# Kernel optimization log

Hardware: AMD Instinct MI355X
Metric: run time of the kernel (lower is better)

## Reference

```python
import jax, jax.numpy as jnp
import numpy as np


def _ortho_matrix(key, d, m):
    # block-orthogonal random matrix with chi-distributed row-norm rescaling
    n_blocks = m // d + (1 if m % d else 0)
    keys = jax.random.split(key, n_blocks + 1)
    blocks = []
    for i in range(m // d):
        q, _ = jnp.linalg.qr(jax.random.normal(keys[i], (d, d), dtype=jnp.float32))
        blocks.append(q)
    rem = m % d
    if rem > 0:
        q, _ = jnp.linalg.qr(jax.random.normal(keys[m // d], (d, d), dtype=jnp.float32))
        blocks.append(q[:, :rem])
    proj = jnp.concatenate(blocks, axis=1)  # [d, m]
    scales = jnp.linalg.norm(jax.random.normal(keys[-1], (m, d), dtype=jnp.float32), axis=1)
    return proj * scales[None, :]


def _feature_map(x, P, eps=1e-6):
    # FAVOR+ positive softmax feature map: [exp(xP - |x|^2/2), exp(-xP - |x|^2/2)]
    proj = x @ P  # [B,N,m]
    xn = 0.5 * jnp.sum(x * x, axis=-1, keepdims=True)
    pos = proj - xn
    neg = -proj - xn
    mx = jnp.maximum(jnp.max(pos, axis=-1, keepdims=True), jnp.max(neg, axis=-1, keepdims=True))
    feats = jnp.concatenate([jnp.exp(pos - mx), jnp.exp(neg - mx)], axis=-1)
    return feats * (2.0 * P.shape[1]) ** -0.5 + eps  # [B,N,2m]


def setup_inputs() -> dict:
    key = jax.random.key(0)
    ks = jax.random.split(key, 16)
    B, C, N = 4, 256, 8192
    da, nb = C // 4, 64
    d_geo, r_geo = 16, 16
    x = jax.random.normal(ks[0], (B, C, N), dtype=jnp.float32)
    pos = jax.random.uniform(ks[1], (B, N, 3), dtype=jnp.float32)
    Wq = jax.random.normal(ks[2], (da, C), dtype=jnp.float32) * (C ** -0.5)
    Wk = jax.random.normal(ks[3], (da, C), dtype=jnp.float32) * (C ** -0.5)
    Wv = jax.random.normal(ks[4], (C, C), dtype=jnp.float32) * (C ** -0.5)
    proj_sm = _ortho_matrix(ks[5], da, nb)  # [da, nb]
    Wg1 = jax.random.normal(ks[6], (d_geo, 3), dtype=jnp.float32) * (3 ** -0.5)
    bg1 = jnp.zeros((d_geo,), dtype=jnp.float32)
    Wg2 = jax.random.normal(ks[7], (d_geo, d_geo), dtype=jnp.float32) * (d_geo ** -0.5)
    bg2 = jnp.zeros((d_geo,), dtype=jnp.float32)
    log_tau = jnp.zeros((), dtype=jnp.float32)
    omega_geo = _ortho_matrix(ks[8], d_geo, r_geo)  # [d_geo, r_geo]
    Wp = jax.random.normal(ks[9], (C, C), dtype=jnp.float32) * (C ** -0.5)
    bn_gamma = jnp.ones((C,), dtype=jnp.float32)
    bn_beta = jnp.zeros((C,), dtype=jnp.float32)
    return {"x": x, "pos": pos, "Wq": Wq, "Wk": Wk, "Wv": Wv, "proj_sm": proj_sm,
            "Wg1": Wg1, "bg1": bg1, "Wg2": Wg2, "bg2": bg2, "log_tau": log_tau,
            "omega_geo": omega_geo, "Wp": Wp, "bn_gamma": bn_gamma, "bn_beta": bn_beta}


def reference(x, pos, Wq, Wk, Wv, proj_sm, Wg1, bg1, Wg2, bg2, log_tau, omega_geo, Wp, bn_gamma, bn_beta):
    eps = 1e-6
    da = Wq.shape[0]
    scale = da ** -0.25
    # 1x1 convs == channel matmuls; transpose to [B,N,*]
    q = jnp.einsum('bcn,oc->bno', x, Wq) * scale
    k = jnp.einsum('bcn,oc->bno', x, Wk) * scale
    v = jnp.einsum('bcn,oc->bno', x, Wv)
    q_p = _feature_map(q, proj_sm, eps)  # [B,N,r_sm]
    k_p = _feature_map(k, proj_sm, eps)
    # GeoRFF: learnable Gaussian RFF on MLP-transformed coordinates
    g = jax.nn.relu(pos @ Wg1.T + bg1) @ Wg2.T + bg2  # [B,N,d_geo]
    tau = jax.nn.softplus(log_tau) + 1e-6
    z = jnp.sqrt(2.0 * tau) * g
    z_proj = z @ omega_geo  # [B,N,r_geo]
    z_norm = 0.5 * jnp.sum(z * z, axis=-1, keepdims=True)
    phi = jnp.exp(z_proj - z_norm) * (omega_geo.shape[1] ** -0.5)  # [B,N,r_geo]
    # outer-product feature combination
    B, N, r_sm = q_p.shape
    r_geo = phi.shape[-1]
    Phi_q = (q_p[..., :, None] * phi[..., None, :]).reshape(B, N, r_sm * r_geo)
    Phi_k = (k_p[..., :, None] * phi[..., None, :]).reshape(B, N, r_sm * r_geo)
    # O(N) linear-attention chain
    kv = jnp.einsum('bnr,bnc->brc', Phi_k, v)         # [B,r,C]
    k_sum = jnp.sum(Phi_k, axis=1)                     # [B,r]
    denom = jnp.einsum('bnr,br->bn', Phi_q, k_sum)[..., None] + eps
    fsa = jnp.einsum('bnr,brc->bnc', Phi_q, kv) / denom  # [B,N,C]
    # offset attention: proj(x - fsa) + x, proj = Conv1x1 -> BN(train stats) -> ReLU
    y = x - jnp.transpose(fsa, (0, 2, 1))  # [B,C,N]
    h = jnp.einsum('bcn,oc->bon', y, Wp)
    mean = jnp.mean(h, axis=(0, 2), keepdims=True)
    var = jnp.var(h, axis=(0, 2), keepdims=True)
    hn = (h - mean) * jax.lax.rsqrt(var + 1e-5) * bn_gamma[None, :, None] + bn_beta[None, :, None]
    return jax.nn.relu(hn) + x
```

## Files before the change

### kernel.cpp

```cpp
#include <hip/hip_runtime.h>
#include <hip/hip_bf16.h>
#include <math.h>

#define BB 4
#define CC 256
#define NN 8192
#define RSM 128
#define RGEO 16

typedef __attribute__((ext_vector_type(8))) short short8v;
typedef __attribute__((ext_vector_type(4))) float f32x4;
typedef __attribute__((ext_vector_type(4))) unsigned int u32x4;

#define MFMA16 __builtin_amdgcn_mfma_f32_16x16x32_bf16

#define P_QP   0ull
#define P_KPT  8388608ull
#define P_PHIR 16777216ull
#define P_PHIT 17825792ull
#define P_XT   18874368ull
#define P_VT   35651584ull
#define P_YNT  35651584ull
#define P_KVT  52428800ull
#define P_KVF  56623104ull
#define P_KSUM 65011712ull
#define P_DEN  65044480ull
#define P_WQK  65175552ull
#define P_WV   65241088ull
#define P_WP   65372160ull
#define P_PSMT 65503232ull
#define P_BN   65511424ull
#define P_H    0ull

__device__ __forceinline__ unsigned short f2bu(float f){
    __hip_bfloat16 h = __float2bfloat16(f);
    return __builtin_bit_cast(unsigned short, h);
}
__device__ __forceinline__ float bu2f(unsigned short u){
    return __builtin_bit_cast(float, ((unsigned int)u) << 16);
}
__device__ __forceinline__ unsigned int pack2(float a, float b){
    return (unsigned int)f2bu(a) | (((unsigned int)f2bu(b)) << 16);
}
__device__ __forceinline__ int swz128(int row, int cb){ return (row*128 + cb) ^ ((row & 7) << 4); }
__device__ __forceinline__ int swz256(int row, int cb){ return (row*256 + cb) ^ ((row & 7) << 4); }

__device__ __forceinline__ void stage64(const unsigned short* __restrict__ g, size_t stride,
                                        char* lds, int t){
    #pragma unroll
    for (int i = 0; i < 2; ++i){
        int id = t + 256*i; int row = id >> 3, q = id & 7;
        short8v v = *(const short8v*)(g + (size_t)row*stride + q*8);
        *(short8v*)(lds + swz128(row, q*16)) = v;
    }
}
__device__ __forceinline__ void stage128(const unsigned short* __restrict__ g, size_t stride,
                                         char* lds, int t){
    #pragma unroll
    for (int i = 0; i < 4; ++i){
        int id = t + 256*i; int row = id >> 3, q = id & 7;
        short8v v = *(const short8v*)(g + (size_t)row*stride + q*8);
        *(short8v*)(lds + swz128(row, q*16)) = v;
    }
}
__device__ __forceinline__ short8v fld(const char* lds, int row, int cb){
    return *(const short8v*)(lds + swz128(row, cb));
}
__device__ __forceinline__ void mfma8(const char* As, const char* Bs, f32x4 acc[2][2],
                                      int wm, int wn, int lr, int lq){
    #pragma unroll
    for (int kk = 0; kk < 2; ++kk){
        short8v a0 = fld(As, wm*32 + lr,      kk*64 + lq*16);
        short8v a1 = fld(As, wm*32 + 16 + lr, kk*64 + lq*16);
        short8v b0 = fld(Bs, wn*32 + lr,      kk*64 + lq*16);
        short8v b1 = fld(Bs, wn*32 + 16 + lr, kk*64 + lq*16);
        acc[0][0] = MFMA16(a0, b0, acc[0][0], 0, 0, 0);
        acc[0][1] = MFMA16(a0, b1, acc[0][1], 0, 0, 0);
        acc[1][0] = MFMA16(a1, b0, acc[1][0], 0, 0, 0);
        acc[1][1] = MFMA16(a1, b1, acc[1][1], 0, 0, 0);
    }
}
__device__ __forceinline__ void mfma16s(const char* As, const char* Bs, f32x4 acc[4][4],
                                        int wm, int wn, int lr, int lq){
    #pragma unroll
    for (int kk = 0; kk < 2; ++kk){
        short8v af[4], bf[4];
        #pragma unroll
        for (int f = 0; f < 4; ++f) af[f] = fld(As, wm*64 + f*16 + lr, kk*64 + lq*16);
        #pragma unroll
        for (int f = 0; f < 4; ++f) bf[f] = fld(Bs, wn*64 + f*16 + lr, kk*64 + lq*16);
        #pragma unroll
        for (int fa = 0; fa < 4; ++fa)
            #pragma unroll
            for (int fb = 0; fb < 4; ++fb)
                acc[fa][fb] = MFMA16(af[fa], bf[fb], acc[fa][fb], 0, 0, 0);
    }
}

__global__ __launch_bounds__(256) void k_prep(const float* __restrict__ Wq, const float* __restrict__ Wk,
    const float* __restrict__ Wv, const float* __restrict__ Wp, const float* __restrict__ Psm,
    unsigned short* __restrict__ Wqk_bf, unsigned short* __restrict__ Wv_bf,
    unsigned short* __restrict__ Wp_bf, unsigned short* __restrict__ Psm_t)
{
    const int tid = blockIdx.x*256 + threadIdx.x;
    const int nth = 64*256;
    for (int i = tid; i < 32768; i += nth){
        int o = i >> 8, c = i & 255;
        Wqk_bf[i] = f2bu(o < 64 ? Wq[o*256 + c] : Wk[(o-64)*256 + c]);
    }
    for (int i = tid; i < 65536; i += nth) Wv_bf[i] = f2bu(Wv[i]);
    for (int i = tid; i < 65536; i += nth) Wp_bf[i] = f2bu(Wp[i]);
    for (int i = tid; i < 4096; i += nth){
        int m = i >> 6, o = i & 63;
        Psm_t[i] = f2bu(Psm[o*64 + m] * 0.35355339059327373f);
    }
}

__global__ __launch_bounds__(256) void k_xt(const float* __restrict__ x, unsigned short* __restrict__ xT)
{
    __shared__ float xs[64][65];
    const int t = threadIdx.x;
    const int b  = blockIdx.x >> 9;
    const int ct = (blockIdx.x >> 7) & 3;
    const int nt = blockIdx.x & 127;
    const int c0 = ct*64, n0 = nt*64;
    #pragma unroll
    for (int i = 0; i < 4; ++i){
        int id = t + 256*i; int row = id >> 4, fq = id & 15;
        f32x4 v = *(const f32x4*)(x + ((size_t)(b*CC + c0 + row))*NN + n0 + fq*4);
        xs[row][fq*4+0] = v[0]; xs[row][fq*4+1] = v[1];
        xs[row][fq*4+2] = v[2]; xs[row][fq*4+3] = v[3];
    }
    __syncthreads();
    #pragma unroll
    for (int i = 0; i < 2; ++i){
        int id = t + 256*i; int n = id >> 3, q = id & 7;
        u32x4 o;
        #pragma unroll
        for (int j2 = 0; j2 < 4; ++j2)
            o[j2] = pack2(xs[q*8 + j2*2][n], xs[q*8 + j2*2+1][n]);
        *(u32x4*)(void*)(xT + ((size_t)(b*NN + n0 + n))*CC + c0 + q*8) = o;
    }
}

__global__ __launch_bounds__(256) void k_wgemm(const unsigned short* __restrict__ A,
    const unsigned short* __restrict__ Bsrc, unsigned short* __restrict__ out, int orows)
{
    __shared__ __align__(16) char As[8192];
    __shared__ __align__(16) char Bs[8192];
    const int t = threadIdx.x;
    const int l = t & 63, w = t >> 6, wm = w >> 1, wn = w & 1, lr = l & 15, lq = l >> 4;
    const int b  = blockIdx.x >> 9;
    const int ct = (blockIdx.x >> 7) & 3;
    const int nt = blockIdx.x & 127;
    const int c0 = ct*64, n0 = nt*64;

    f32x4 acc[2][2] = {};
    for (int ks = 0; ks < 4; ++ks){
        stage64(A + (size_t)c0*256 + ks*64, 256, As, t);
        stage64(Bsrc + ((size_t)(b*NN + n0))*256 + ks*64, 256, Bs, t);
        __syncthreads();
        mfma8(As, Bs, acc, wm, wn, lr, lq);
        __syncthreads();
    }
    #pragma unroll
    for (int mi = 0; mi < 2; ++mi)
        #pragma unroll
        for (int ni = 0; ni < 2; ++ni)
            #pragma unroll
            for (int r = 0; r < 4; ++r){
                int c = c0 + wm*32 + mi*16 + lq*4 + r;
                int n = n0 + wn*32 + ni*16 + lr;
                out[((size_t)(b*orows + c))*NN + n] = f2bu(acc[mi][ni][r]);
            }
}

__global__ __launch_bounds__(256) void k_qk(const unsigned short* __restrict__ Wqk,
    const unsigned short* __restrict__ xT, const unsigned short* __restrict__ Psm_t,
    unsigned short* __restrict__ qp, unsigned short* __restrict__ kp_t)
{
    __shared__ __align__(16) char As[16384];
    __shared__ __align__(16) char Bs[8192];
    __shared__ __align__(16) char Ts[16384];
    __shared__ __align__(16) char Ps[8192];
    const int t = threadIdx.x;
    const int l = t & 63, w = t >> 6, wm = w >> 1, wn = w & 1, lr = l & 15, lq = l >> 4;
    const int b  = blockIdx.x >> 7;
    const int nt = blockIdx.x & 127;
    const int n0 = nt*64;

    stage64(Psm_t, 64, Ps, t);

    f32x4 acc[4][2] = {};
    for (int ks = 0; ks < 4; ++ks){
        #pragma unroll
        for (int i = 0; i < 4; ++i){
            int id = t + 256*i; int row = id >> 3, q = id & 7;
            short8v v = *(const short8v*)(Wqk + (size_t)row*256 + ks*64 + q*8);
            *(short8v*)(As + swz128(row, q*16)) = v;
        }
        stage64(xT + ((size_t)(b*NN + n0))*256 + ks*64, 256, Bs, t);
        __syncthreads();
        #pragma unroll
        for (int kk = 0; kk < 2; ++kk){
            short8v b0 = fld(Bs, wn*32 + lr,      kk*64 + lq*16);
            short8v b1 = fld(Bs, wn*32 + 16 + lr, kk*64 + lq*16);
            #pragma unroll
            for (int mi = 0; mi < 4; ++mi){
                short8v a = fld(As, wm*64 + mi*16 + lr, kk*64 + lq*16);
                acc[mi][0] = MFMA16(a, b0, acc[mi][0], 0, 0, 0);
                acc[mi][1] = MFMA16(a, b1, acc[mi][1], 0, 0, 0);
            }
        }
        __syncthreads();
    }
    #pragma unroll
    for (int mi = 0; mi < 4; ++mi)
        #pragma unroll
        for (int ni = 0; ni < 2; ++ni){
            int op = (wm*64 + mi*16 + lq*4)*2;
            int nrow = wn*32 + ni*16 + lr;
            *(unsigned int*)(Ts + swz256(nrow, op))     = pack2(acc[mi][ni][0], acc[mi][ni][1]);
            *(unsigned int*)(Ts + swz256(nrow, op + 4)) = pack2(acc[mi][ni][2], acc[mi][ni][3]);
        }
    __syncthreads();

    const float inv128 = 0.08838834764831845f;
    for (int p = 0; p < 2; ++p){
        f32x4 ac[4] = {};
        #pragma unroll
        for (int kk = 0; kk < 2; ++kk){
            short8v bf = *(const short8v*)(Ts + swz256(w*16 + lr, p*128 + kk*64 + lq*16));
            #pragma unroll
            for (int mi = 0; mi < 4; ++mi){
                short8v a = *(const short8v*)(Ps + swz128(mi*16 + lr, kk*64 + lq*16));
                ac[mi] = MFMA16(a, bf, ac[mi], 0, 0, 0);
            }
        }
        float mx = 0.f;
        #pragma unroll
        for (int mi = 0; mi < 4; ++mi)
            #pragma unroll
            for (int r = 0; r < 4; ++r) mx = fmaxf(mx, fabsf(ac[mi][r]));
        mx = fmaxf(mx, __shfl_xor(mx, 16));
        mx = fmaxf(mx, __shfl_xor(mx, 32));
        const int n = n0 + w*16 + lr;
        if (p == 0){
            unsigned short* qr = qp + ((size_t)(b*NN + n))*RSM;
            #pragma unroll
            for (int mi = 0; mi < 4; ++mi){
                float e0 = __expf( ac[mi][0]-mx)*inv128 + 1e-6f;
                float e1 = __expf( ac[mi][1]-mx)*inv128 + 1e-6f;
                float e2 = __expf( ac[mi][2]-mx)*inv128 + 1e-6f;
                float e3 = __expf( ac[mi][3]-mx)*inv128 + 1e-6f;
                float g0 = __expf(-ac[mi][0]-mx)*inv128 + 1e-6f;
                float g1 = __expf(-ac[mi][1]-mx)*inv128 + 1e-6f;
                float g2 = __expf(-ac[mi][2]-mx)*inv128 + 1e-6f;
                float g3 = __expf(-ac[mi][3]-mx)*inv128 + 1e-6f;
                int i0 = mi*16 + lq*4;
                uint2 pu; pu.x = pack2(e0, e1); pu.y = pack2(e2, e3);
                uint2 nu; nu.x = pack2(g0, g1); nu.y = pack2(g2, g3);
                *(uint2*)(void*)(qr + i0)      = pu;
                *(uint2*)(void*)(qr + 64 + i0) = nu;
            }
        } else {
            unsigned short* kb = kp_t + (size_t)(b*RSM)*NN + n;
            #pragma unroll
            for (int mi = 0; mi < 4; ++mi){
                int i0 = mi*16 + lq*4;
                #pragma unroll
                for (int r = 0; r < 4; ++r){
                    kb[(size_t)(i0 + r)*NN]      = f2bu(__expf( ac[mi][r]-mx)*inv128 + 1e-6f);
                    kb[(size_t)(i0 + r + 64)*NN] = f2bu(__expf(-ac[mi][r]-mx)*inv128 + 1e-6f);
                }
            }
        }
    }
}

__global__ __launch_bounds__(256) void k_phi(const float* __restrict__ pos,
    const float* __restrict__ Wg1, const float* __restrict__ bg1,
    const float* __restrict__ Wg2, const float* __restrict__ bg2,
    const float* __restrict__ log_tau, const float* __restrict__ omega,
    unsigned short* __restrict__ phi_row, unsigned short* __restrict__ phi_t)
{
    const int t = threadIdx.x;
    const int b = blockIdx.x >> 5;
    const int n = ((blockIdx.x & 31) << 8) + t;
    const float* pp = pos + ((size_t)(b*NN + n))*3;
    const float p0 = pp[0], p1 = pp[1], p2 = pp[2];
    float hb[16];
    #pragma unroll
    for (int i = 0; i < 16; ++i)
        hb[i] = fmaxf(0.f, fmaf(Wg1[i*3+0], p0, fmaf(Wg1[i*3+1], p1, fmaf(Wg1[i*3+2], p2, bg1[i]))));
    const float tau = log1pf(__expf(log_tau[0])) + 1e-6f;
    const float sc  = sqrtf(2.f*tau);
    float z[16]; float zn = 0.f;
    #pragma unroll
    for (int i = 0; i < 16; ++i){
        float g = bg2[i];
        #pragma unroll
        for (int j = 0; j < 16; ++j) g = fmaf(Wg2[i*16+j], hb[j], g);
        z[i] = sc*g; zn = fmaf(z[i], z[i], zn);
    }
    zn *= 0.5f;
    float val[16];
    #pragma unroll
    for (int m = 0; m < 16; ++m){
        float s = 0.f;
        #pragma unroll
        for (int i = 0; i < 16; ++i) s = fmaf(z[i], omega[i*16+m], s);
        val[m] = __expf(s - zn)*0.25f;
    }
    unsigned short* pr = phi_row + ((size_t)(b*NN + n))*16;
    u32x4 o0, o1;
    #pragma unroll
    for (int j2 = 0; j2 < 4; ++j2){
        o0[j2] = pack2(val[j2*2], val[j2*2+1]);
        o1[j2] = pack2(val[8+j2*2], val[8+j2*2+1]);
    }
    *(u32x4*)(void*)pr = o0;
    *(u32x4*)(void*)(pr + 8) = o1;
    #pragma unroll
    for (int m = 0; m < 16; ++m)
        phi_t[((size_t)(b*RGEO + m))*NN + n] = f2bu(val[m]);
}

__global__ __launch_bounds__(256) void k_kv(const unsigned short* __restrict__ kp_t,
    const unsigned short* __restrict__ phi_t, const unsigned short* __restrict__ v_t,
    float* __restrict__ kv_f32, float* __restrict__ ksum)
{
    __shared__ __align__(16) char As[16384];
    __shared__ __align__(16) char Bs[16384];
    const int t = threadIdx.x;
    const int l = t & 63, w = t >> 6, wm = w >> 1, wn = w & 1, lr = l & 15, lq = l >> 4;
    const int bid = blockIdx.x;
    const int rt  = bid & 15;
    const int ct  = (bid >> 4) & 1;
    const int ksl = (bid >> 5) & 7;
    const int b   = bid >> 8;
    const int c0 = ct*128, r0 = rt*128;

    const int brow = t >> 1, half = t & 1;
    const int rg = r0 + brow;
    const unsigned short* kpr = kp_t + ((size_t)(b*RSM  + (rg >> 4)))*NN;
    const unsigned short* phr = phi_t + ((size_t)(b*RGEO + (rg & 15)))*NN;
    float ksacc = 0.f;

    f32x4 acc[4][4] = {};
    for (int ks = 0; ks < 16; ++ks){
        const int nk = ksl*1024 + ks*64;
        stage128(v_t + ((size_t)(b*CC + c0))*NN + nk, NN, As, t);
        {
            const int nb = nk + half*32;
            #pragma unroll
            for (int c4 = 0; c4 < 2; ++c4){
                short8v k0 = *(const short8v*)(kpr + nb + c4*16);
                short8v k1 = *(const short8v*)(kpr + nb + c4*16 + 8);
                short8v p0 = *(const short8v*)(phr + nb + c4*16);
                short8v p1 = *(const short8v*)(phr + nb + c4*16 + 8);
                float pr0[8], pr1[8];
                #pragma unroll
                for (int e = 0; e < 8; ++e){
                    pr0[e] = bu2f((unsigned short)k0[e])*bu2f((unsigned short)p0[e]);
                    pr1[e] = bu2f((unsigned short)k1[e])*bu2f((unsigned short)p1[e]);
                }
                if (ct == 0){
                    #pragma unroll
                    for (int e = 0; e < 8; ++e) ksacc += pr0[e] + pr1[e];
                }
                u32x4 o0, o1;
                #pragma unroll
                for (int j2 = 0; j2 < 4; ++j2){
                    o0[j2] = pack2(pr0[j2*2], pr0[j2*2+1]);
                    o1[j2] = pack2(pr1[j2*2], pr1[j2*2+1]);
                }
                *(u32x4*)(Bs + swz128(brow, half*64 + c4*32))      = o0;
                *(u32x4*)(Bs + swz128(brow, half*64 + c4*32 + 16)) = o1;
            }
        }
        __syncthreads();
        mfma16s(As, Bs, acc, wm, wn, lr, lq);
        __syncthreads();
    }
    #pragma unroll
    for (int fa = 0; fa < 4; ++fa)
        #pragma unroll
        for (int fb = 0; fb < 4; ++fb)
            #pragma unroll
            for (int e = 0; e < 4; ++e){
                int c = c0 + wm*64 + fa*16 + lq*4 + e;
                int r = r0 + wn*64 + fb*16 + lr;
                atomicAdd(&kv_f32[((size_t)(b*CC + c))*2048 + r], acc[fa][fb][e]);
            }
    if (ct == 0){
        float o = __shfl_xor(ksacc, 1);
        if (half == 0) atomicAdd(&ksum[b*2048 + rg], ksacc + o);
    }
}

__global__ __launch_bounds__(256) void k_kvred(const float* __restrict__ kv_f32,
    unsigned short* __restrict__ kv_t)
{
    const size_t i = ((size_t)blockIdx.x*256 + threadIdx.x)*4;
    f32x4 v = *(const f32x4*)(kv_f32 + i);
    uint2 o; o.x = pack2(v[0], v[1]); o.y = pack2(v[2], v[3]);
    *(uint2*)(void*)(kv_t + i) = o;
}

__global__ __launch_bounds__(256) void k_denom(const unsigned short* __restrict__ qp,
    const unsigned short* __restrict__ phi_row, const float* __restrict__ ksum,
    float* __restrict__ den)
{
    __shared__ float ks[2048];
    const int t = threadIdx.x;
    const int b = blockIdx.x >> 5;
    const int n = ((blockIdx.x & 31) << 8) + t;
    const float* ksrc = ksum + b*2048;
    #pragma unroll
    for (int i = 0; i < 8; ++i){ int idx = t + 256*i; ks[idx] = ksrc[idx]; }
    __syncthreads();
    float phf[16];
    {
        const unsigned short* pr = phi_row + ((size_t)(b*NN + n))*16;
        short8v a = *(const short8v*)pr;
        short8v c = *(const short8v*)(pr + 8);
        #pragma unroll
        for (int j = 0; j < 8; ++j){ phf[j] = bu2f((unsigned short)a[j]); phf[8+j] = bu2f((unsigned short)c[j]); }
    }
    const unsigned short* qr = qp + ((size_t)(b*NN + n))*RSM;
    float acc = 0.f;
    for (int i = 0; i < 128; i += 8){
        short8v qv = *(const short8v*)(qr + i);
        #pragma unroll
        for (int ii = 0; ii < 8; ++ii){
            const float* kk = &ks[(i + ii)*16];
            float s = 0.f;
            #pragma unroll
            for (int j = 0; j < 16; ++j) s = fmaf(phf[j], kk[j], s);
            acc = fmaf(bu2f((unsigned short)qv[ii]), s, acc);
        }
    }
    den[b*NN + n] = acc + 1e-6f;
}

__global__ __launch_bounds__(256) void k_fsa(const unsigned short* __restrict__ kv_t,
    const unsigned short* __restrict__ qp, const unsigned short* __restrict__ phi_row,
    const float* __restrict__ den, const unsigned short* __restrict__ xT,
    unsigned short* __restrict__ y_nt)
{
    __shared__ __align__(16) char Sm[32768];
    char* As = Sm;
    char* Bs = Sm + 16384;
    const int t = threadIdx.x;
    const int l = t & 63, w = t >> 6, wm = w >> 1, wn = w & 1, lr = l & 15, lq = l >> 4;
    const int nt = blockIdx.x & 63;
    const int ct = (blockIdx.x >> 6) & 1;
    const int b  = blockIdx.x >> 7;
    const int c0 = ct*128, n0 = nt*128;

    const int brow = t >> 1, half = t & 1;
    float phf[16];
    {
        const unsigned short* pr = phi_row + ((size_t)(b*NN + n0 + brow))*16;
        short8v a = *(const short8v*)pr;
        short8v c = *(const short8v*)(pr + 8);
        #pragma unroll
        for (int j = 0; j < 8; ++j){ phf[j] = bu2f((unsigned short)a[j]); phf[8+j] = bu2f((unsigned short)c[j]); }
    }
    const unsigned short* qrow = qp + ((size_t)(b*NN + n0 + brow))*RSM;

    f32x4 acc[4][4] = {};
    for (int ks = 0; ks < 32; ++ks){
        const int rk = ks*64;
        stage128(kv_t + ((size_t)(b*CC + c0))*2048 + rk, 2048, As, t);
        {
            const int ib = (rk >> 4) + half*2;
            const float q0 = bu2f(qrow[ib]);
            const float q1 = bu2f(qrow[ib + 1]);
            u32x4 oa, ob;
            #pragma unroll
            for (int j2 = 0; j2 < 4; ++j2){
                oa[j2] = pack2(q0*phf[j2*2],     q0*phf[j2*2+1]);
                ob[j2] = pack2(q0*phf[8+j2*2],   q0*phf[8+j2*2+1]);
            }
            *(u32x4*)(Bs + swz128(brow, half*64))      = oa;
            *(u32x4*)(Bs + swz128(brow, half*64 + 16)) = ob;
            #pragma unroll
            for (int j2 = 0; j2 < 4; ++j2){
                oa[j2] = pack2(q1*phf[j2*2],     q1*phf[j2*2+1]);
                ob[j2] = pack2(q1*phf[8+j2*2],   q1*phf[8+j2*2+1]);
            }
            *(u32x4*)(Bs + swz128(brow, half*64 + 32)) = oa;
            *(u32x4*)(Bs + swz128(brow, half*64 + 48)) = ob;
        }
        __syncthreads();
        mfma16s(As, Bs, acc, wm, wn, lr, lq);
        __syncthreads();
    }
    float rd[4];
    #pragma unroll
    for (int fb = 0; fb < 4; ++fb)
        rd[fb] = 1.0f / den[(size_t)b*NN + n0 + wn*64 + fb*16 + lr];
    #pragma unroll
    for (int fa = 0; fa < 4; ++fa)
        #pragma unroll
        for (int fb = 0; fb < 4; ++fb){
            int nrow = wn*64 + fb*16 + lr;
            int cb   = (wm*64 + fa*16 + lq*4)*2;
            *(unsigned int*)(Sm + swz256(nrow, cb))     = pack2(acc[fa][fb][0]*rd[fb], acc[fa][fb][1]*rd[fb]);
            *(unsigned int*)(Sm + swz256(nrow, cb + 4)) = pack2(acc[fa][fb][2]*rd[fb], acc[fa][fb][3]*rd[fb]);
        }
    __syncthreads();
    #pragma unroll
    for (int i = 0; i < 8; ++i){
        int id = t + 256*i; int row = id >> 4, q = id & 15;
        short8v fs = *(const short8v*)(Sm + swz256(row, q*16));
        short8v xv = *(const short8v*)(xT + ((size_t)(b*NN + n0 + row))*CC + c0 + q*8);
        u32x4 o;
        #pragma unroll
        for (int j2 = 0; j2 < 4; ++j2){
            float y0 = bu2f((unsigned short)xv[j2*2])   - bu2f((unsigned short)fs[j2*2]);
            float y1 = bu2f((unsigned short)xv[j2*2+1]) - bu2f((unsigned short)fs[j2*2+1]);
            o[j2] = pack2(y0, y1);
        }
        *(u32x4*)(void*)(y_nt + ((size_t)(b*NN + n0 + row))*CC + c0 + q*8) = o;
    }
}

__global__ __launch_bounds__(256) void k_bnstat(const unsigned short* __restrict__ h,
    const float* __restrict__ gamma, const float* __restrict__ beta, float* __restrict__ bn)
{
    __shared__ float s1[256], s2[256];
    const int t = threadIdx.x, c = blockIdx.x;
    float a1 = 0.f, a2 = 0.f;
    for (int b = 0; b < 4; ++b){
        const unsigned short* hr = h + ((size_t)(b*CC + c))*NN;
        #pragma unroll
        for (int i = 0; i < 4; ++i){
            short8v v = *(const short8v*)(hr + (t + i*256)*8);
            #pragma unroll
            for (int j = 0; j < 8; ++j){ float f = bu2f((unsigned short)v[j]); a1 += f; a2 = fmaf(f, f, a2); }
        }
    }
    s1[t] = a1; s2[t] = a2; __syncthreads();
    for (int st = 128; st > 0; st >>= 1){
        if (t < st){ s1[t] += s1[t + st]; s2[t] += s2[t + st]; }
        __syncthreads();
    }
    if (t == 0){
        float inv = 1.f/32768.f;
        float mean = s1[0]*inv, var = s2[0]*inv - mean*mean;
        float sc = gamma[c]*rsqrtf(var + 1e-5f);
        bn[512 + c] = sc; bn[768 + c] = fmaf(-mean, sc, beta[c]);
    }
}

__global__ __launch_bounds__(256) void k_apply(const unsigned short* __restrict__ h,
    const float* __restrict__ x, const float* __restrict__ bn, float* __restrict__ out)
{
    const size_t tot8 = (size_t)BB*CC*NN/8;
    for (size_t i = (size_t)blockIdx.x*256 + threadIdx.x; i < tot8; i += 2048*256){
        int c = (int)((i >> 10) & 255);
        float s = bn[512 + c], bb = bn[768 + c];
        short8v hv = *(const short8v*)(h + i*8);
        f32x4 x0 = *(const f32x4*)(x + i*8);
        f32x4 x1 = *(const f32x4*)(x + i*8 + 4);
        f32x4 o0, o1;
        #pragma unroll
        for (int j = 0; j < 4; ++j){
            o0[j] = fmaxf(fmaf(bu2f((unsigned short)hv[j]),     s, bb), 0.f) + x0[j];
            o1[j] = fmaxf(fmaf(bu2f((unsigned short)hv[4 + j]), s, bb), 0.f) + x1[j];
        }
        *(f32x4*)(out + i*8)     = o0;
        *(f32x4*)(out + i*8 + 4) = o1;
    }
}

extern "C" void kernel_launch(void* const* d_in, const int* in_sizes, int n_in,
                              void* d_out, int out_size, void* d_ws, size_t ws_size,
                              hipStream_t stream)
{
    (void)in_sizes; (void)n_in; (void)out_size; (void)ws_size;
    const float* x       = (const float*)d_in[0];
    const float* pos     = (const float*)d_in[1];
    const float* Wq      = (const float*)d_in[2];
    const float* Wk      = (const float*)d_in[3];
    const float* Wv      = (const float*)d_in[4];
    const float* Psm     = (const float*)d_in[5];
    const float* Wg1     = (const float*)d_in[6];
    const float* bg1     = (const float*)d_in[7];
    const float* Wg2     = (const float*)d_in[8];
    const float* bg2     = (const float*)d_in[9];
    const float* log_tau = (const float*)d_in[10];
    const float* omega   = (const float*)d_in[11];
    const float* Wp      = (const float*)d_in[12];
    const float* gamma   = (const float*)d_in[13];
    const float* beta    = (const float*)d_in[14];
    char* W = (char*)d_ws;
    float* out = (float*)d_out;

    unsigned short* qp    = (unsigned short*)(W + P_QP);
    unsigned short* kp_t  = (unsigned short*)(W + P_KPT);
    unsigned short* phir  = (unsigned short*)(W + P_PHIR);
    unsigned short* phit  = (unsigned short*)(W + P_PHIT);
    unsigned short* xT    = (unsigned short*)(W + P_XT);
    unsigned short* v_t   = (unsigned short*)(W + P_VT);
    unsigned short* y_nt  = (unsigned short*)(W + P_YNT);
    unsigned short* kv_t  = (unsigned short*)(W + P_KVT);
    float*          kvf   = (float*)(W + P_KVF);
    float*          ksum  = (float*)(W + P_KSUM);
    float*          den   = (float*)(W + P_DEN);
    unsigned short* Wqk_b = (unsigned short*)(W + P_WQK);
    unsigned short* Wv_b  = (unsigned short*)(W + P_WV);
    unsigned short* Wp_b  = (unsigned short*)(W + P_WP);
    unsigned short* Psm_t = (unsigned short*)(W + P_PSMT);
    float*          bn    = (float*)(W + P_BN);
    unsigned short* hbuf  = (unsigned short*)(W + P_H);

    hipMemsetAsync(W + P_KVF, 0, 8421376, stream);
    k_prep  <<<  64, 256, 0, stream>>>(Wq, Wk, Wv, Wp, Psm, Wqk_b, Wv_b, Wp_b, Psm_t);
    k_xt    <<<2048, 256, 0, stream>>>(x, xT);
    k_wgemm <<<2048, 256, 0, stream>>>(Wv_b, xT, v_t, 256);
    k_qk    <<< 512, 256, 0, stream>>>(Wqk_b, xT, Psm_t, qp, kp_t);
    k_phi   <<< 128, 256, 0, stream>>>(pos, Wg1, bg1, Wg2, bg2, log_tau, omega, phir, phit);
    k_kv    <<<1024, 256, 0, stream>>>(kp_t, phit, v_t, kvf, ksum);
    k_kvred <<<2048, 256, 0, stream>>>(kvf, kv_t);
    k_denom <<< 128, 256, 0, stream>>>(qp, phir, ksum, den);
    k_fsa   <<< 512, 256, 0, stream>>>(kv_t, qp, phir, den, xT, y_nt);
    k_wgemm <<<2048, 256, 0, stream>>>(Wp_b, y_nt, hbuf, 256);
    k_bnstat<<< 256, 256, 0, stream>>>(hbuf, gamma, beta, bn);
    k_apply <<<2048, 256, 0, stream>>>(hbuf, x, bn, out);
}
```

Measured before the change: 330.0 us.

## Prefetch operand tiles into registers and shrink tiles in k_kv and k_fsa

k_kv and k_fsa now load the next k-step's V/kv tile and the feature products into registers while the current tile is multiplied. Each iteration drops one barrier and overlaps global loads with MFMA work. k_kv doubles its split-K slices to 16 and launches 2048 blocks. k_fsa halves the N tile to 64 with a 4x2 MFMA fragment layout and launches 1024 blocks, so more blocks can run at once. The cost is higher register pressure and more partial-sum traffic in the split-K reduction.

```diff
diff --git a/kernel.cpp b/kernel.cpp
--- a/kernel.cpp
+++ b/kernel.cpp
@@ -45,19 +45,17 @@
 __device__ __forceinline__ int swz128(int row, int cb){ return (row*128 + cb) ^ ((row & 7) << 4); }
 __device__ __forceinline__ int swz256(int row, int cb){ return (row*256 + cb) ^ ((row & 7) << 4); }
 
+__device__ __forceinline__ unsigned int bmul2(unsigned int uk, unsigned int up, float& ksacc){
+    float lo = __builtin_bit_cast(float, uk << 16) * __builtin_bit_cast(float, up << 16);
+    float hi = __builtin_bit_cast(float, uk & 0xffff0000u) * __builtin_bit_cast(float, up & 0xffff0000u);
+    ksacc += lo + hi;
+    return pack2(lo, hi);
+}
+
 __device__ __forceinline__ void stage64(const unsigned short* __restrict__ g, size_t stride,
                                         char* lds, int t){
     #pragma unroll
     for (int i = 0; i < 2; ++i){
-        int id = t + 256*i; int row = id >> 3, q = id & 7;
-        short8v v = *(const short8v*)(g + (size_t)row*stride + q*8);
-        *(short8v*)(lds + swz128(row, q*16)) = v;
-    }
-}
-__device__ __forceinline__ void stage128(const unsigned short* __restrict__ g, size_t stride,
-                                         char* lds, int t){
-    #pragma unroll
-    for (int i = 0; i < 4; ++i){
         int id = t + 256*i; int row = id >> 3, q = id & 7;
         short8v v = *(const short8v*)(g + (size_t)row*stride + q*8);
         *(short8v*)(lds + swz128(row, q*16)) = v;
@@ -93,6 +91,22 @@
         for (int fa = 0; fa < 4; ++fa)
             #pragma unroll
             for (int fb = 0; fb < 4; ++fb)
+                acc[fa][fb] = MFMA16(af[fa], bf[fb], acc[fa][fb], 0, 0, 0);
+    }
+}
+__device__ __forceinline__ void mfma4x2(const char* As, const char* Bs, f32x4 acc[4][2],
+                                        int wm, int wn, int lr, int lq){
+    #pragma unroll
+    for (int kk = 0; kk < 2; ++kk){
+        short8v af[4], bf[2];
+        #pragma unroll
+        for (int f = 0; f < 4; ++f) af[f] = fld(As, wm*64 + f*16 + lr, kk*64 + lq*16);
+        #pragma unroll
+        for (int f = 0; f < 2; ++f) bf[f] = fld(Bs, wn*32 + f*16 + lr, kk*64 + lq*16);
+        #pragma unroll
+        for (int fa = 0; fa < 4; ++fa)
+            #pragma unroll
+            for (int fb = 0; fb < 2; ++fb)
                 acc[fa][fb] = MFMA16(af[fa], bf[fb], acc[fa][fb], 0, 0, 0);
     }
 }
@@ -337,51 +351,59 @@
     const int bid = blockIdx.x;
     const int rt  = bid & 15;
     const int ct  = (bid >> 4) & 1;
-    const int ksl = (bid >> 5) & 7;
-    const int b   = bid >> 8;
+    const int ksl = (bid >> 5) & 15;
+    const int b   = bid >> 9;
     const int c0 = ct*128, r0 = rt*128;
 
+    const int arow = t >> 3, aq = t & 7;
     const int brow = t >> 1, half = t & 1;
     const int rg = r0 + brow;
     const unsigned short* kpr = kp_t + ((size_t)(b*RSM  + (rg >> 4)))*NN;
     const unsigned short* phr = phi_t + ((size_t)(b*RGEO + (rg & 15)))*NN;
+    const unsigned short* vb  = v_t + ((size_t)(b*CC + c0))*NN;
     float ksacc = 0.f;
 
+    short8v vA[4];
+    unsigned int ob[16];
+    int nk = ksl*512;
+
+    #pragma unroll
+    for (int i = 0; i < 4; ++i)
+        vA[i] = *(const short8v*)(vb + (size_t)(arow + 32*i)*NN + nk + aq*8);
+    #pragma unroll
+    for (int g2 = 0; g2 < 4; ++g2){
+        u32x4 uk = __builtin_bit_cast(u32x4, *(const short8v*)(kpr + nk + half*32 + g2*8));
+        u32x4 up = __builtin_bit_cast(u32x4, *(const short8v*)(phr + nk + half*32 + g2*8));
+        #pragma unroll
+        for (int j = 0; j < 4; ++j) ob[g2*4 + j] = bmul2(uk[j], up[j], ksacc);
+    }
+
     f32x4 acc[4][4] = {};
-    for (int ks = 0; ks < 16; ++ks){
-        const int nk = ksl*1024 + ks*64;
-        stage128(v_t + ((size_t)(b*CC + c0))*NN + nk, NN, As, t);
-        {
-            const int nb = nk + half*32;
-            #pragma unroll
-            for (int c4 = 0; c4 < 2; ++c4){
-                short8v k0 = *(const short8v*)(kpr + nb + c4*16);
-                short8v k1 = *(const short8v*)(kpr + nb + c4*16 + 8);
-                short8v p0 = *(const short8v*)(phr + nb + c4*16);
-                short8v p1 = *(const short8v*)(phr + nb + c4*16 + 8);
-                float pr0[8], pr1[8];
+    for (int ks = 0; ks < 8; ++ks){
+        __syncthreads();
+        #pragma unroll
+        for (int i = 0; i < 4; ++i)
+            *(short8v*)(As + swz128(arow + 32*i, aq*16)) = vA[i];
+        #pragma unroll
+        for (int g2 = 0; g2 < 4; ++g2){
+            u32x4 o; o[0]=ob[g2*4]; o[1]=ob[g2*4+1]; o[2]=ob[g2*4+2]; o[3]=ob[g2*4+3];
+            *(u32x4*)(Bs + swz128(brow, half*64 + g2*16)) = o;
+        }
+        if (ks < 7){
+            nk += 64;
+            #pragma unroll
+            for (int i = 0; i < 4; ++i)
+                vA[i] = *(const short8v*)(vb + (size_t)(arow + 32*i)*NN + nk + aq*8);
+            #pragma unroll
+            for (int g2 = 0; g2 < 4; ++g2){
+                u32x4 uk = __builtin_bit_cast(u32x4, *(const short8v*)(kpr + nk + half*32 + g2*8));
+                u32x4 up = __builtin_bit_cast(u32x4, *(const short8v*)(phr + nk + half*32 + g2*8));
                 #pragma unroll
-                for (int e = 0; e < 8; ++e){
-                    pr0[e] = bu2f((unsigned short)k0[e])*bu2f((unsigned short)p0[e]);
-                    pr1[e] = bu2f((unsigned short)k1[e])*bu2f((unsigned short)p1[e]);
-                }
-                if (ct == 0){
-                    #pragma unroll
-                    for (int e = 0; e < 8; ++e) ksacc += pr0[e] + pr1[e];
-                }
-                u32x4 o0, o1;
-                #pragma unroll
-                for (int j2 = 0; j2 < 4; ++j2){
-                    o0[j2] = pack2(pr0[j2*2], pr0[j2*2+1]);
-                    o1[j2] = pack2(pr1[j2*2], pr1[j2*2+1]);
-                }
-                *(u32x4*)(Bs + swz128(brow, half*64 + c4*32))      = o0;
-                *(u32x4*)(Bs + swz128(brow, half*64 + c4*32 + 16)) = o1;
+                for (int j = 0; j < 4; ++j) ob[g2*4 + j] = bmul2(uk[j], up[j], ksacc);
             }
         }
         __syncthreads();
         mfma16s(As, Bs, acc, wm, wn, lr, lq);
-        __syncthreads();
     }
     #pragma unroll
     for (int fa = 0; fa < 4; ++fa)
@@ -449,17 +471,18 @@
     const float* __restrict__ den, const unsigned short* __restrict__ xT,
     unsigned short* __restrict__ y_nt)
 {
-    __shared__ __align__(16) char Sm[32768];
+    __shared__ __align__(16) char Sm[24576];
     char* As = Sm;
     char* Bs = Sm + 16384;
     const int t = threadIdx.x;
     const int l = t & 63, w = t >> 6, wm = w >> 1, wn = w & 1, lr = l & 15, lq = l >> 4;
-    const int nt = blockIdx.x & 63;
-    const int ct = (blockIdx.x >> 6) & 1;
-    const int b  = blockIdx.x >> 7;
-    const int c0 = ct*128, n0 = nt*128;
-
-    const int brow = t >> 1, half = t & 1;
+    const int nt = blockIdx.x & 127;
+    const int ct = (blockIdx.x >> 7) & 1;
+    const int b  = blockIdx.x >> 8;
+    const int c0 = ct*128, n0 = nt*64;
+
+    const int arow = t >> 3, aq = t & 7;
+    const int brow = t >> 2, quarter = t & 3;
     float phf[16];
     {
         const unsigned short* pr = phi_row + ((size_t)(b*NN + n0 + brow))*16;
@@ -469,51 +492,57 @@
         for (int j = 0; j < 8; ++j){ phf[j] = bu2f((unsigned short)a[j]); phf[8+j] = bu2f((unsigned short)c[j]); }
     }
     const unsigned short* qrow = qp + ((size_t)(b*NN + n0 + brow))*RSM;
-
-    f32x4 acc[4][4] = {};
+    const unsigned short* kvb  = kv_t + ((size_t)(b*CC + c0))*2048;
+
+    short8v vA[4];
+    float qv;
+    int rk = 0;
+    #pragma unroll
+    for (int i = 0; i < 4; ++i)
+        vA[i] = *(const short8v*)(kvb + (size_t)(arow + 32*i)*2048 + rk + aq*8);
+    qv = bu2f(qrow[(rk >> 4) + quarter]);
+
+    f32x4 acc[4][2] = {};
     for (int ks = 0; ks < 32; ++ks){
-        const int rk = ks*64;
-        stage128(kv_t + ((size_t)(b*CC + c0))*2048 + rk, 2048, As, t);
-        {
-            const int ib = (rk >> 4) + half*2;
-            const float q0 = bu2f(qrow[ib]);
-            const float q1 = bu2f(qrow[ib + 1]);
-            u32x4 oa, ob;
-            #pragma unroll
-            for (int j2 = 0; j2 < 4; ++j2){
-                oa[j2] = pack2(q0*phf[j2*2],     q0*phf[j2*2+1]);
-                ob[j2] = pack2(q0*phf[8+j2*2],   q0*phf[8+j2*2+1]);
-            }
-            *(u32x4*)(Bs + swz128(brow, half*64))      = oa;
-            *(u32x4*)(Bs + swz128(brow, half*64 + 16)) = ob;
-            #pragma unroll
-            for (int j2 = 0; j2 < 4; ++j2){
-                oa[j2] = pack2(q1*phf[j2*2],     q1*phf[j2*2+1]);
-                ob[j2] = pack2(q1*phf[8+j2*2],   q1*phf[8+j2*2+1]);
-            }
-            *(u32x4*)(Bs + swz128(brow, half*64 + 32)) = oa;
-            *(u32x4*)(Bs + swz128(brow, half*64 + 48)) = ob;
-        }
-        __syncthreads();
-        mfma16s(As, Bs, acc, wm, wn, lr, lq);
-        __syncthreads();
-    }
-    float rd[4];
-    #pragma unroll
-    for (int fb = 0; fb < 4; ++fb)
-        rd[fb] = 1.0f / den[(size_t)b*NN + n0 + wn*64 + fb*16 + lr];
+        u32x4 o0, o1;
+        #pragma unroll
+        for (int j2 = 0; j2 < 4; ++j2){
+            o0[j2] = pack2(qv*phf[j2*2],     qv*phf[j2*2+1]);
+            o1[j2] = pack2(qv*phf[8+j2*2],   qv*phf[8+j2*2+1]);
+        }
+        __syncthreads();
+        #pragma unroll
+        for (int i = 0; i < 4; ++i)
+            *(short8v*)(As + swz128(arow + 32*i, aq*16)) = vA[i];
+        *(u32x4*)(Bs + swz128(brow, quarter*32))      = o0;
+        *(u32x4*)(Bs + swz128(brow, quarter*32 + 16)) = o1;
+        if (ks < 31){
+            rk += 64;
+            #pragma unroll
+            for (int i = 0; i < 4; ++i)
+                vA[i] = *(const short8v*)(kvb + (size_t)(arow + 32*i)*2048 + rk + aq*8);
+            qv = bu2f(qrow[(rk >> 4) + quarter]);
+        }
+        __syncthreads();
+        mfma4x2(As, Bs, acc, wm, wn, lr, lq);
+    }
+    __syncthreads();
+    float rd[2];
+    #pragma unroll
+    for (int fb = 0; fb < 2; ++fb)
+        rd[fb] = 1.0f / den[(size_t)b*NN + n0 + wn*32 + fb*16 + lr];
     #pragma unroll
     for (int fa = 0; fa < 4; ++fa)
         #pragma unroll
-        for (int fb = 0; fb < 4; ++fb){
-            int nrow = wn*64 + fb*16 + lr;
+        for (int fb = 0; fb < 2; ++fb){
+            int nrow = wn*32 + fb*16 + lr;
             int cb   = (wm*64 + fa*16 + lq*4)*2;
             *(unsigned int*)(Sm + swz256(nrow, cb))     = pack2(acc[fa][fb][0]*rd[fb], acc[fa][fb][1]*rd[fb]);
             *(unsigned int*)(Sm + swz256(nrow, cb + 4)) = pack2(acc[fa][fb][2]*rd[fb], acc[fa][fb][3]*rd[fb]);
         }
     __syncthreads();
     #pragma unroll
-    for (int i = 0; i < 8; ++i){
+    for (int i = 0; i < 4; ++i){
         int id = t + 256*i; int row = id >> 4, q = id & 15;
         short8v fs = *(const short8v*)(Sm + swz256(row, q*16));
         short8v xv = *(const short8v*)(xT + ((size_t)(b*NN + n0 + row))*CC + c0 + q*8);
@@ -624,10 +653,10 @@
     k_wgemm <<<2048, 256, 0, stream>>>(Wv_b, xT, v_t, 256);
     k_qk    <<< 512, 256, 0, stream>>>(Wqk_b, xT, Psm_t, qp, kp_t);
     k_phi   <<< 128, 256, 0, stream>>>(pos, Wg1, bg1, Wg2, bg2, log_tau, omega, phir, phit);
-    k_kv    <<<1024, 256, 0, stream>>>(kp_t, phit, v_t, kvf, ksum);
+    k_kv    <<<2048, 256, 0, stream>>>(kp_t, phit, v_t, kvf, ksum);
     k_kvred <<<2048, 256, 0, stream>>>(kvf, kv_t);
     k_denom <<< 128, 256, 0, stream>>>(qp, phir, ksum, den);
-    k_fsa   <<< 512, 256, 0, stream>>>(kv_t, qp, phir, den, xT, y_nt);
+    k_fsa   <<<1024, 256, 0, stream>>>(kv_t, qp, phir, den, xT, y_nt);
     k_wgemm <<<2048, 256, 0, stream>>>(Wp_b, y_nt, hbuf, 256);
     k_bnstat<<< 256, 256, 0, stream>>>(hbuf, gamma, beta, bn);
     k_apply <<<2048, 256, 0, stream>>>(hbuf, x, bn, out);
```

Measured after the change: 353.3 us. 1.07x slower.
